# Kernel tuning notes

Measured on AMD Instinct MI355X. Metric: run time of the kernel, lower is better.

Reference implementation:

```python
import jax, jax.numpy as jnp
import numpy as np

K_HOPS = 4  # matches init kwarg K


def setup_inputs() -> dict:
    key = jax.random.key(0)
    ks = jax.random.split(key, 6)
    B, N, Fin, Fout = 32, 128, 64, 64
    x = jax.random.normal(ks[0], (B, N, Fin), dtype=jnp.float32)
    P = jax.random.normal(ks[1], (N, N), dtype=jnp.float32)
    Bb = jax.random.normal(ks[2], (N, 1), dtype=jnp.float32)
    Q = jax.random.normal(ks[3], (Fin, Fin), dtype=jnp.float32)
    T = jax.random.normal(ks[4], (Fin, N * Fin), dtype=jnp.float32)
    U = jax.random.normal(ks[5], (Fin, Fout), dtype=jnp.float32)
    return {"x": x, "P": P, "Bb": Bb, "Q": Q, "T": T, "U": U}


def reference(x, P, Bb, Q, T, U):
    B, N, Fin = x.shape
    # adjacency generation: O = P x + b, G = relu((O Q) T)
    O = jnp.matmul(P, x) + Bb                      # (B, N, Fin)
    G = jax.nn.relu(jnp.matmul(jnp.matmul(O, Q), T))  # (B, N, N*Fin)
    G = G.reshape(B, N, N, Fin).transpose(0, 3, 1, 2)  # (B, Fin, N, N)
    # degree normalization: A = diag(1/sqrt(colsum)) G diag(1/sqrt(rowsum))
    Dii = jnp.sqrt(jnp.sum(G, axis=-2))            # (B, Fin, N) column sums
    Djj = jnp.sqrt(jnp.sum(G, axis=-1))            # (B, Fin, N) row sums
    A = G / Dii[..., :, None] / Djj[..., None, :]  # (B, Fin, N, N)
    # K-hop power series: Asum = I + A + ... + A^{K-1}
    AA = jnp.broadcast_to(jnp.eye(N, dtype=x.dtype), A.shape)
    Asum = jnp.zeros_like(A)
    for _ in range(K_HOPS - 1):
        Asum = Asum + AA
        AA = jnp.matmul(A, AA)
    Asum = Asum + AA
    # propagate each feature channel: X[b,n,f] = sum_m Asum[b,f,n,m] x[b,m,f]
    Xf = jnp.einsum('bfnm,bmf->bnf', Asum, x)      # (B, N, Fin)
    return jnp.matmul(Xf, U)                       # (B, N, Fout)
```

## Files before the change

kernel.cpp:

```cpp
#include <hip/hip_runtime.h>


typedef __attribute__((ext_vector_type(8))) short short8v;
typedef __attribute__((ext_vector_type(4))) float f32x4;

#define WS_THE 0u
#define WS_TLE (1u << 20)
#define WS_XT  (2u << 20)
#define WS_TRE (3u << 20)
#define WS_OQH (3u << 20)
#define WS_OQL ((3u << 20) + (512u << 10))
#define WS_XFT (4u << 20)

__device__ __forceinline__ void split_bf16(float a, unsigned& hi, unsigned& lo) {
  unsigned ha = __float_as_uint(a) & 0xffff0000u;
  float d = a - __uint_as_float(ha);
  unsigned la = __float_as_uint(d) & 0xffff0000u;
  hi = ha; lo = la;
}

__global__ __launch_bounds__(256) void iag_k0_transpose(
    const float* __restrict__ T, const float* __restrict__ x,
    float* __restrict__ Tre, float* __restrict__ xT) {
  __shared__ float tile[64 * 65];
  int bi = blockIdx.x, tid = threadIdx.x;
  const float* src;
  float* dstbase;
  int fstride;
  if (bi < 128) {
    int k = bi >> 1, half = bi & 1;
    src = T + k * 8192 + half * 64 * 64;
    dstbase = Tre + k * 128 + half * 64;
    fstride = 8192;
  } else {
    int j = bi - 128;
    int b = j >> 1, half = j & 1;
    src = x + b * 8192 + half * 64 * 64;
    dstbase = xT + b * 8192 + half * 64;
    fstride = 128;
  }
  for (int idx = tid; idx < 4096; idx += 256) {
    int c = idx & 63, r = idx >> 6;
    tile[r * 65 + c] = src[idx];
  }
  __syncthreads();
  for (int idx = tid; idx < 4096; idx += 256) {
    int r = idx & 63, c = idx >> 6;
    dstbase[c * fstride + r] = tile[r * 65 + c];
  }
}

__global__ __launch_bounds__(256) void iag_k0b_split(
    const float* __restrict__ Tre, unsigned short* __restrict__ The,
    unsigned short* __restrict__ Tle) {
  __shared__ float tile[64 * 129];
  int f = blockIdx.x, tid = threadIdx.x;
  const float* src = Tre + f * 8192;
  for (int idx = tid; idx < 8192; idx += 256) {
    int k = idx >> 7, m = idx & 127;
    tile[k * 129 + m] = src[idx];
  }
  __syncthreads();
  int m = tid >> 1, kc = (tid & 1) * 32;
  unsigned hw[16], lw[16];
#pragma unroll
  for (int kk = 0; kk < 32; kk += 2) {
    float a0 = tile[(kc + kk) * 129 + m];
    float a1 = tile[(kc + kk + 1) * 129 + m];
    unsigned h0, l0, h1, l1;
    split_bf16(a0, h0, l0);
    split_bf16(a1, h1, l1);
    hw[kk >> 1] = (h0 >> 16) | h1;
    lw[kk >> 1] = (l0 >> 16) | l1;
  }
  uint4* dh = (uint4*)(The + f * 8192 + m * 64 + kc);
  uint4* dl = (uint4*)(Tle + f * 8192 + m * 64 + kc);
#pragma unroll
  for (int i = 0; i < 4; ++i) {
    dh[i] = make_uint4(hw[4 * i], hw[4 * i + 1], hw[4 * i + 2], hw[4 * i + 3]);
    dl[i] = make_uint4(lw[4 * i], lw[4 * i + 1], lw[4 * i + 2], lw[4 * i + 3]);
  }
}

__global__ __launch_bounds__(256) void iag_k1_oq(
    const float* __restrict__ x, const float* __restrict__ P,
    const float* __restrict__ Q, const float* __restrict__ Bb,
    unsigned short* __restrict__ OQh, unsigned short* __restrict__ OQl) {
  __shared__ __align__(16) float x_s[128 * 64];
  __shared__ float ptile[32 * 129];
  __shared__ __align__(16) float Q_s[64 * 64];
  __shared__ __align__(16) float OcT[64 * 32];
  int b = blockIdx.y, r0 = blockIdx.x * 32, tid = threadIdx.x;

  const float4* xg = (const float4*)(x + b * 8192);
  float4* xs4 = (float4*)x_s;
  for (int idx = tid; idx < 2048; idx += 256) xs4[idx] = xg[idx];
  for (int idx = tid; idx < 4096; idx += 256) {
    int nl = idx >> 7, m = idx & 127;
    ptile[nl * 129 + m] = P[(r0 + nl) * 128 + m];
  }
  const float4* qg = (const float4*)Q;
  float4* qs4 = (float4*)Q_s;
  for (int idx = tid; idx < 1024; idx += 256) qs4[idx] = qg[idx];
  __syncthreads();

  {
    int nl = tid & 31, k0 = (tid >> 5) * 8;
    float bias = Bb[r0 + nl];
    float a[8];
#pragma unroll
    for (int j = 0; j < 8; ++j) a[j] = bias;
#pragma unroll 4
    for (int m = 0; m < 128; ++m) {
      float p = ptile[nl * 129 + m];
      float4 x0 = xs4[m * 16 + (k0 >> 2)];
      float4 x1 = xs4[m * 16 + (k0 >> 2) + 1];
      a[0] += p * x0.x; a[1] += p * x0.y; a[2] += p * x0.z; a[3] += p * x0.w;
      a[4] += p * x1.x; a[5] += p * x1.y; a[6] += p * x1.z; a[7] += p * x1.w;
    }
#pragma unroll
    for (int j = 0; j < 8; ++j) OcT[(k0 + j) * 32 + nl] = a[j];
  }
  __syncthreads();
  {
    int nl = tid >> 3, j0 = (tid & 7) * 8;
    float c[8];
#pragma unroll
    for (int i = 0; i < 8; ++i) c[i] = 0.f;
    const float4* q4 = (const float4*)Q_s;
#pragma unroll 4
    for (int k = 0; k < 64; ++k) {
      float o = OcT[k * 32 + nl];
      float4 q0 = q4[k * 16 + (j0 >> 2)];
      float4 q1 = q4[k * 16 + (j0 >> 2) + 1];
      c[0] += o * q0.x; c[1] += o * q0.y; c[2] += o * q0.z; c[3] += o * q0.w;
      c[4] += o * q1.x; c[5] += o * q1.y; c[6] += o * q1.z; c[7] += o * q1.w;
    }
    unsigned hw[4], lw[4];
#pragma unroll
    for (int j = 0; j < 8; j += 2) {
      unsigned h0, l0, h1, l1;
      split_bf16(c[j], h0, l0);
      split_bf16(c[j + 1], h1, l1);
      hw[j >> 1] = (h0 >> 16) | h1;
      lw[j >> 1] = (l0 >> 16) | l1;
    }
    int n = r0 + nl;
    *(uint4*)(OQh + b * 8192 + n * 64 + j0) = make_uint4(hw[0], hw[1], hw[2], hw[3]);
    *(uint4*)(OQl + b * 8192 + n * 64 + j0) = make_uint4(lw[0], lw[1], lw[2], lw[3]);
  }
}

__global__ __launch_bounds__(256) void iag_k2_graph(
    const unsigned short* __restrict__ OQh, const unsigned short* __restrict__ OQl,
    const unsigned short* __restrict__ The, const unsigned short* __restrict__ Tle,
    const float* __restrict__ xT, float* __restrict__ Xft) {
  __shared__ unsigned short Ah[128 * 72], Al[128 * 72];
  __shared__ unsigned short Bh[128 * 72], Bl[128 * 72];
  __shared__ float red[4 * 128];
  __shared__ float invc[128], invr[128];
  __shared__ float wvb[2][128];
  int f = blockIdx.x, b = blockIdx.y, tid = threadIdx.x;

  {
    const unsigned short* sAh = OQh + b * 8192;
    const unsigned short* sAl = OQl + b * 8192;
    const unsigned short* sBh = The + f * 8192;
    const unsigned short* sBl = Tle + f * 8192;
#pragma unroll
    for (int it = 0; it < 4; ++it) {
      int c = tid + it * 256;
      int row = c >> 3, slot = c & 7;
      int so = row * 64 + slot * 8, dofs = row * 72 + slot * 8;
      *(uint4*)(Ah + dofs) = *(const uint4*)(sAh + so);
      *(uint4*)(Al + dofs) = *(const uint4*)(sAl + so);
      *(uint4*)(Bh + dofs) = *(const uint4*)(sBh + so);
      *(uint4*)(Bl + dofs) = *(const uint4*)(sBl + so);
    }
  }
  if (tid < 128) wvb[0][tid] = xT[(b * 64 + f) * 128 + tid];
  __syncthreads();

  int lane = tid & 63, w = tid >> 6;
  int li = lane & 15, lk = lane >> 4;

  short8v ah[2][2], al[2][2];
#pragma unroll
  for (int nt = 0; nt < 2; ++nt)
#pragma unroll
    for (int kh = 0; kh < 2; ++kh) {
      int off = (w * 32 + nt * 16 + li) * 72 + kh * 32 + lk * 8;
      ah[nt][kh] = *(const short8v*)((const short*)Ah + off);
      al[nt][kh] = *(const short8v*)((const short*)Al + off);
    }

  f32x4 acc[2][8];
#pragma unroll
  for (int nt = 0; nt < 2; ++nt)
#pragma unroll
    for (int mt = 0; mt < 8; ++mt) acc[nt][mt] = (f32x4){0.f, 0.f, 0.f, 0.f};

#pragma unroll
  for (int mt = 0; mt < 8; ++mt) {
    int off = (mt * 16 + li) * 72 + lk * 8;
    short8v bh0 = *(const short8v*)((const short*)Bh + off);
    short8v bh1 = *(const short8v*)((const short*)Bh + off + 32);
    short8v bl0 = *(const short8v*)((const short*)Bl + off);
    short8v bl1 = *(const short8v*)((const short*)Bl + off + 32);
#pragma unroll
    for (int nt = 0; nt < 2; ++nt) {
      f32x4 a = acc[nt][mt];
      a = __builtin_amdgcn_mfma_f32_16x16x32_bf16(ah[nt][0], bh0, a, 0, 0, 0);
      a = __builtin_amdgcn_mfma_f32_16x16x32_bf16(ah[nt][1], bh1, a, 0, 0, 0);
      a = __builtin_amdgcn_mfma_f32_16x16x32_bf16(ah[nt][0], bl0, a, 0, 0, 0);
      a = __builtin_amdgcn_mfma_f32_16x16x32_bf16(ah[nt][1], bl1, a, 0, 0, 0);
      a = __builtin_amdgcn_mfma_f32_16x16x32_bf16(al[nt][0], bh0, a, 0, 0, 0);
      a = __builtin_amdgcn_mfma_f32_16x16x32_bf16(al[nt][1], bh1, a, 0, 0, 0);
      acc[nt][mt] = a;
    }
  }

#pragma unroll
  for (int nt = 0; nt < 2; ++nt)
#pragma unroll
    for (int mt = 0; mt < 8; ++mt)
#pragma unroll
      for (int r = 0; r < 4; ++r) acc[nt][mt][r] = fmaxf(acc[nt][mt][r], 0.f);

#pragma unroll
  for (int mt = 0; mt < 8; ++mt) {
    float cs = 0.f;
#pragma unroll
    for (int nt = 0; nt < 2; ++nt)
#pragma unroll
      for (int r = 0; r < 4; ++r) cs += acc[nt][mt][r];
    cs += __shfl_xor(cs, 16);
    cs += __shfl_xor(cs, 32);
    if (lk == 0) red[w * 128 + mt * 16 + li] = cs;
  }
  {
    float rs[2][4];
#pragma unroll
    for (int nt = 0; nt < 2; ++nt)
#pragma unroll
      for (int r = 0; r < 4; ++r) {
        float s = 0.f;
#pragma unroll
        for (int mt = 0; mt < 8; ++mt) s += acc[nt][mt][r];
        rs[nt][r] = s;
      }
#pragma unroll
    for (int d = 1; d <= 8; d <<= 1)
#pragma unroll
      for (int nt = 0; nt < 2; ++nt)
#pragma unroll
        for (int r = 0; r < 4; ++r) rs[nt][r] += __shfl_xor(rs[nt][r], d);
    if (li == 0) {
#pragma unroll
      for (int nt = 0; nt < 2; ++nt)
#pragma unroll
        for (int r = 0; r < 4; ++r)
          invr[w * 32 + nt * 16 + lk * 4 + r] = rs[nt][r];
    }
  }
  __syncthreads();
  if (tid < 128) {
    float csum = red[tid] + red[128 + tid] + red[256 + tid] + red[384 + tid];
    invc[tid] = 1.0f / sqrtf(csum);
    invr[tid] = 1.0f / sqrtf(invr[tid]);
  }
  __syncthreads();

  {
    float icf[2][4], irf[8];
#pragma unroll
    for (int nt = 0; nt < 2; ++nt)
#pragma unroll
      for (int r = 0; r < 4; ++r) icf[nt][r] = invc[w * 32 + nt * 16 + lk * 4 + r];
#pragma unroll
    for (int mt = 0; mt < 8; ++mt) irf[mt] = invr[mt * 16 + li];
#pragma unroll
    for (int nt = 0; nt < 2; ++nt)
#pragma unroll
      for (int mt = 0; mt < 8; ++mt)
#pragma unroll
        for (int r = 0; r < 4; ++r) acc[nt][mt][r] *= icf[nt][r] * irf[mt];
  }

  float sv[2][4];
#pragma unroll
  for (int nt = 0; nt < 2; ++nt)
#pragma unroll
    for (int r = 0; r < 4; ++r) sv[nt][r] = wvb[0][w * 32 + nt * 16 + lk * 4 + r];
  int cur = 0;
  for (int h = 0; h < 3; ++h) {
    float wr[8];
#pragma unroll
    for (int mt = 0; mt < 8; ++mt) wr[mt] = wvb[cur][mt * 16 + li];
    float p[2][4];
#pragma unroll
    for (int nt = 0; nt < 2; ++nt)
#pragma unroll
      for (int r = 0; r < 4; ++r) {
        float s = 0.f;
#pragma unroll
        for (int mt = 0; mt < 8; ++mt) s += acc[nt][mt][r] * wr[mt];
        p[nt][r] = s;
      }
#pragma unroll
    for (int d = 1; d <= 8; d <<= 1)
#pragma unroll
      for (int nt = 0; nt < 2; ++nt)
#pragma unroll
        for (int r = 0; r < 4; ++r) p[nt][r] += __shfl_xor(p[nt][r], d);
#pragma unroll
    for (int nt = 0; nt < 2; ++nt)
#pragma unroll
      for (int r = 0; r < 4; ++r) sv[nt][r] += p[nt][r];
    if (li == 0) {
#pragma unroll
      for (int nt = 0; nt < 2; ++nt)
#pragma unroll
        for (int r = 0; r < 4; ++r)
          wvb[cur ^ 1][w * 32 + nt * 16 + lk * 4 + r] = p[nt][r];
    }
    __syncthreads();
    cur ^= 1;
  }
  if (li == 0) {
#pragma unroll
    for (int nt = 0; nt < 2; ++nt)
#pragma unroll
      for (int r = 0; r < 4; ++r)
        Xft[(b * 64 + f) * 128 + w * 32 + nt * 16 + lk * 4 + r] = sv[nt][r];
  }
}

__global__ __launch_bounds__(256) void iag_k3_out(
    const float* __restrict__ Xft, const float* __restrict__ U,
    float* __restrict__ out) {
  __shared__ float Xf_s[64 * 36];
  __shared__ __align__(16) float U_s[64 * 64];
  int b = blockIdx.y, n0 = blockIdx.x * 32, tid = threadIdx.x;
  for (int c = tid; c < 512; c += 256) {
    int ff = c >> 3, s = c & 7;
    float4 v = *(const float4*)(Xft + (b * 64 + ff) * 128 + n0 + s * 4);
    *(float4*)(Xf_s + ff * 36 + s * 4) = v;
  }
  const float4* ug = (const float4*)U;
  float4* us = (float4*)U_s;
  for (int c = tid; c < 1024; c += 256) us[c] = ug[c];
  __syncthreads();

  int j0 = (tid & 15) * 4, nl0 = (tid >> 4) * 2;
  float a0[4] = {0.f, 0.f, 0.f, 0.f}, a1[4] = {0.f, 0.f, 0.f, 0.f};
  const float4* u4 = (const float4*)U_s;
#pragma unroll 4
  for (int ff = 0; ff < 64; ++ff) {
    float4 u = u4[ff * 16 + (j0 >> 2)];
    float xa = Xf_s[ff * 36 + nl0];
    float xb = Xf_s[ff * 36 + nl0 + 1];
    a0[0] += xa * u.x; a0[1] += xa * u.y; a0[2] += xa * u.z; a0[3] += xa * u.w;
    a1[0] += xb * u.x; a1[1] += xb * u.y; a1[2] += xb * u.z; a1[3] += xb * u.w;
  }
  *(float4*)(out + b * 8192 + (n0 + nl0) * 64 + j0) =
      make_float4(a0[0], a0[1], a0[2], a0[3]);
  *(float4*)(out + b * 8192 + (n0 + nl0 + 1) * 64 + j0) =
      make_float4(a1[0], a1[1], a1[2], a1[3]);
}

extern "C" void kernel_launch(void* const* d_in, const int* in_sizes, int n_in,
                              void* d_out, int out_size, void* d_ws, size_t ws_size,
                              hipStream_t stream) {
  const float* x  = (const float*)d_in[0];
  const float* P  = (const float*)d_in[1];
  const float* Bb = (const float*)d_in[2];
  const float* Q  = (const float*)d_in[3];
  const float* T  = (const float*)d_in[4];
  const float* U  = (const float*)d_in[5];
  char* wsb = (char*)d_ws;
  unsigned short* The = (unsigned short*)(wsb + WS_THE);
  unsigned short* Tle = (unsigned short*)(wsb + WS_TLE);
  float* xT  = (float*)(wsb + WS_XT);
  float* Tre = (float*)(wsb + WS_TRE);
  unsigned short* OQh = (unsigned short*)(wsb + WS_OQH);
  unsigned short* OQl = (unsigned short*)(wsb + WS_OQL);
  float* Xft = (float*)(wsb + WS_XFT);

  iag_k0_transpose<<<192, 256, 0, stream>>>(T, x, Tre, xT);
  iag_k0b_split<<<64, 256, 0, stream>>>(Tre, The, Tle);
  iag_k1_oq<<<dim3(4, 32), 256, 0, stream>>>(x, P, Q, Bb, OQh, OQl);
  iag_k2_graph<<<dim3(64, 32), 256, 0, stream>>>(OQh, OQl, The, Tle, xT, Xft);
  iag_k3_out<<<dim3(4, 32), 256, 0, stream>>>(Xft, U, (float*)d_out);
}
```

Before: 123.2 us.

## Fuse preprocessing kernels and load MFMA operands directly from global memory

Merges the T transpose, the bf16 hi/lo split and the OQ computation into one preprocessing kernel, so the launch sequence drops from five kernels to three and the intermediate Tre and xT buffers go away. The graph kernel now reads its bf16 MFMA fragments straight from global memory instead of staging them in LDS, which removes the shared-memory copy and one barrier. It also gains a launch-bounds occupancy hint. The cost is repeated global or L2 fragment loads per wave and a strided global read of x for the propagation vector.

```diff
diff --git a/kernel.cpp b/kernel.cpp
--- a/kernel.cpp
+++ b/kernel.cpp
@@ -6,11 +6,9 @@
 
 #define WS_THE 0u
 #define WS_TLE (1u << 20)
-#define WS_XT  (2u << 20)
-#define WS_TRE (3u << 20)
-#define WS_OQH (3u << 20)
-#define WS_OQL ((3u << 20) + (512u << 10))
-#define WS_XFT (4u << 20)
+#define WS_OQH (2u << 20)
+#define WS_OQL ((2u << 20) + (512u << 10))
+#define WS_XFT (3u << 20)
 
 __device__ __forceinline__ void split_bf16(float a, unsigned& hi, unsigned& lo) {
   unsigned ha = __float_as_uint(a) & 0xffff0000u;
@@ -19,179 +17,139 @@
   hi = ha; lo = la;
 }
 
-__global__ __launch_bounds__(256) void iag_k0_transpose(
+__global__ __launch_bounds__(256) void iag_kpre(
     const float* __restrict__ T, const float* __restrict__ x,
-    float* __restrict__ Tre, float* __restrict__ xT) {
-  __shared__ float tile[64 * 65];
+    const float* __restrict__ P, const float* __restrict__ Q,
+    const float* __restrict__ Bb,
+    unsigned short* __restrict__ The, unsigned short* __restrict__ Tle,
+    unsigned short* __restrict__ OQh, unsigned short* __restrict__ OQl) {
+  __shared__ __align__(16) char smem[73856];
   int bi = blockIdx.x, tid = threadIdx.x;
-  const float* src;
-  float* dstbase;
-  int fstride;
-  if (bi < 128) {
-    int k = bi >> 1, half = bi & 1;
-    src = T + k * 8192 + half * 64 * 64;
-    dstbase = Tre + k * 128 + half * 64;
-    fstride = 8192;
+
+  if (bi < 64) {
+    float* tile = (float*)smem;
+    int m0 = bi * 2;
+    for (int idx = tid; idx < 8192; idx += 256) {
+      int k = idx >> 7, j = idx & 127;
+      tile[k * 129 + j] = T[k * 8192 + m0 * 64 + j];
+    }
+    __syncthreads();
+    int p = tid >> 1, kc = (tid & 1) * 32;
+    int fj = p & 63, ml = p >> 6;
+    int j = ml * 64 + fj;
+    unsigned hw[16], lw[16];
+#pragma unroll
+    for (int kk = 0; kk < 32; kk += 2) {
+      float a0 = tile[(kc + kk) * 129 + j];
+      float a1 = tile[(kc + kk + 1) * 129 + j];
+      unsigned h0, l0, h1, l1;
+      split_bf16(a0, h0, l0);
+      split_bf16(a1, h1, l1);
+      hw[kk >> 1] = (h0 >> 16) | h1;
+      lw[kk >> 1] = (l0 >> 16) | l1;
+    }
+    uint4* dh = (uint4*)(The + fj * 8192 + (m0 + ml) * 64 + kc);
+    uint4* dl = (uint4*)(Tle + fj * 8192 + (m0 + ml) * 64 + kc);
+#pragma unroll
+    for (int i = 0; i < 4; ++i) {
+      dh[i] = make_uint4(hw[4 * i], hw[4 * i + 1], hw[4 * i + 2], hw[4 * i + 3]);
+      dl[i] = make_uint4(lw[4 * i], lw[4 * i + 1], lw[4 * i + 2], lw[4 * i + 3]);
+    }
   } else {
-    int j = bi - 128;
-    int b = j >> 1, half = j & 1;
-    src = x + b * 8192 + half * 64 * 64;
-    dstbase = xT + b * 8192 + half * 64;
-    fstride = 128;
-  }
-  for (int idx = tid; idx < 4096; idx += 256) {
-    int c = idx & 63, r = idx >> 6;
-    tile[r * 65 + c] = src[idx];
-  }
-  __syncthreads();
-  for (int idx = tid; idx < 4096; idx += 256) {
-    int r = idx & 63, c = idx >> 6;
-    dstbase[c * fstride + r] = tile[r * 65 + c];
-  }
-}
-
-__global__ __launch_bounds__(256) void iag_k0b_split(
-    const float* __restrict__ Tre, unsigned short* __restrict__ The,
-    unsigned short* __restrict__ Tle) {
-  __shared__ float tile[64 * 129];
-  int f = blockIdx.x, tid = threadIdx.x;
-  const float* src = Tre + f * 8192;
-  for (int idx = tid; idx < 8192; idx += 256) {
-    int k = idx >> 7, m = idx & 127;
-    tile[k * 129 + m] = src[idx];
-  }
-  __syncthreads();
-  int m = tid >> 1, kc = (tid & 1) * 32;
-  unsigned hw[16], lw[16];
-#pragma unroll
-  for (int kk = 0; kk < 32; kk += 2) {
-    float a0 = tile[(kc + kk) * 129 + m];
-    float a1 = tile[(kc + kk + 1) * 129 + m];
-    unsigned h0, l0, h1, l1;
-    split_bf16(a0, h0, l0);
-    split_bf16(a1, h1, l1);
-    hw[kk >> 1] = (h0 >> 16) | h1;
-    lw[kk >> 1] = (l0 >> 16) | l1;
-  }
-  uint4* dh = (uint4*)(The + f * 8192 + m * 64 + kc);
-  uint4* dl = (uint4*)(Tle + f * 8192 + m * 64 + kc);
-#pragma unroll
-  for (int i = 0; i < 4; ++i) {
-    dh[i] = make_uint4(hw[4 * i], hw[4 * i + 1], hw[4 * i + 2], hw[4 * i + 3]);
-    dl[i] = make_uint4(lw[4 * i], lw[4 * i + 1], lw[4 * i + 2], lw[4 * i + 3]);
-  }
-}
-
-__global__ __launch_bounds__(256) void iag_k1_oq(
-    const float* __restrict__ x, const float* __restrict__ P,
-    const float* __restrict__ Q, const float* __restrict__ Bb,
-    unsigned short* __restrict__ OQh, unsigned short* __restrict__ OQl) {
-  __shared__ __align__(16) float x_s[128 * 64];
-  __shared__ float ptile[32 * 129];
-  __shared__ __align__(16) float Q_s[64 * 64];
-  __shared__ __align__(16) float OcT[64 * 32];
-  int b = blockIdx.y, r0 = blockIdx.x * 32, tid = threadIdx.x;
-
-  const float4* xg = (const float4*)(x + b * 8192);
-  float4* xs4 = (float4*)x_s;
-  for (int idx = tid; idx < 2048; idx += 256) xs4[idx] = xg[idx];
-  for (int idx = tid; idx < 4096; idx += 256) {
-    int nl = idx >> 7, m = idx & 127;
-    ptile[nl * 129 + m] = P[(r0 + nl) * 128 + m];
-  }
-  const float4* qg = (const float4*)Q;
-  float4* qs4 = (float4*)Q_s;
-  for (int idx = tid; idx < 1024; idx += 256) qs4[idx] = qg[idx];
-  __syncthreads();
-
-  {
-    int nl = tid & 31, k0 = (tid >> 5) * 8;
-    float bias = Bb[r0 + nl];
-    float a[8];
-#pragma unroll
-    for (int j = 0; j < 8; ++j) a[j] = bias;
+    float* x_s   = (float*)smem;
+    float* ptile = x_s + 128 * 64;
+    float* Q_s   = ptile + 32 * 129;
+    float* OcT   = Q_s + 64 * 64;
+    int jb = bi - 64;
+    int b = jb >> 2, r0 = (jb & 3) * 32;
+
+    const float4* xg = (const float4*)(x + b * 8192);
+    float4* xs4 = (float4*)x_s;
+    for (int idx = tid; idx < 2048; idx += 256) xs4[idx] = xg[idx];
+    for (int idx = tid; idx < 4096; idx += 256) {
+      int nl = idx >> 7, m = idx & 127;
+      ptile[nl * 129 + m] = P[(r0 + nl) * 128 + m];
+    }
+    const float4* qg = (const float4*)Q;
+    float4* qs4 = (float4*)Q_s;
+    for (int idx = tid; idx < 1024; idx += 256) qs4[idx] = qg[idx];
+    __syncthreads();
+
+    {
+      int nl = tid & 31, k0 = (tid >> 5) * 8;
+      float bias = Bb[r0 + nl];
+      float a[8];
+#pragma unroll
+      for (int j = 0; j < 8; ++j) a[j] = bias;
 #pragma unroll 4
-    for (int m = 0; m < 128; ++m) {
-      float p = ptile[nl * 129 + m];
-      float4 x0 = xs4[m * 16 + (k0 >> 2)];
-      float4 x1 = xs4[m * 16 + (k0 >> 2) + 1];
-      a[0] += p * x0.x; a[1] += p * x0.y; a[2] += p * x0.z; a[3] += p * x0.w;
-      a[4] += p * x1.x; a[5] += p * x1.y; a[6] += p * x1.z; a[7] += p * x1.w;
-    }
-#pragma unroll
-    for (int j = 0; j < 8; ++j) OcT[(k0 + j) * 32 + nl] = a[j];
-  }
-  __syncthreads();
-  {
-    int nl = tid >> 3, j0 = (tid & 7) * 8;
-    float c[8];
-#pragma unroll
-    for (int i = 0; i < 8; ++i) c[i] = 0.f;
-    const float4* q4 = (const float4*)Q_s;
+      for (int m = 0; m < 128; ++m) {
+        float p = ptile[nl * 129 + m];
+        float4 x0 = xs4[m * 16 + (k0 >> 2)];
+        float4 x1 = xs4[m * 16 + (k0 >> 2) + 1];
+        a[0] += p * x0.x; a[1] += p * x0.y; a[2] += p * x0.z; a[3] += p * x0.w;
+        a[4] += p * x1.x; a[5] += p * x1.y; a[6] += p * x1.z; a[7] += p * x1.w;
+      }
+#pragma unroll
+      for (int j = 0; j < 8; ++j) OcT[(k0 + j) * 32 + nl] = a[j];
+    }
+    __syncthreads();
+    {
+      int nl = tid >> 3, j0 = (tid & 7) * 8;
+      float c[8];
+#pragma unroll
+      for (int i = 0; i < 8; ++i) c[i] = 0.f;
+      const float4* q4 = (const float4*)Q_s;
 #pragma unroll 4
-    for (int k = 0; k < 64; ++k) {
-      float o = OcT[k * 32 + nl];
-      float4 q0 = q4[k * 16 + (j0 >> 2)];
-      float4 q1 = q4[k * 16 + (j0 >> 2) + 1];
-      c[0] += o * q0.x; c[1] += o * q0.y; c[2] += o * q0.z; c[3] += o * q0.w;
-      c[4] += o * q1.x; c[5] += o * q1.y; c[6] += o * q1.z; c[7] += o * q1.w;
-    }
-    unsigned hw[4], lw[4];
-#pragma unroll
-    for (int j = 0; j < 8; j += 2) {
-      unsigned h0, l0, h1, l1;
-      split_bf16(c[j], h0, l0);
-      split_bf16(c[j + 1], h1, l1);
-      hw[j >> 1] = (h0 >> 16) | h1;
-      lw[j >> 1] = (l0 >> 16) | l1;
-    }
-    int n = r0 + nl;
-    *(uint4*)(OQh + b * 8192 + n * 64 + j0) = make_uint4(hw[0], hw[1], hw[2], hw[3]);
-    *(uint4*)(OQl + b * 8192 + n * 64 + j0) = make_uint4(lw[0], lw[1], lw[2], lw[3]);
-  }
-}
-
-__global__ __launch_bounds__(256) void iag_k2_graph(
+      for (int k = 0; k < 64; ++k) {
+        float o = OcT[k * 32 + nl];
+        float4 q0 = q4[k * 16 + (j0 >> 2)];
+        float4 q1 = q4[k * 16 + (j0 >> 2) + 1];
+        c[0] += o * q0.x; c[1] += o * q0.y; c[2] += o * q0.z; c[3] += o * q0.w;
+        c[4] += o * q1.x; c[5] += o * q1.y; c[6] += o * q1.z; c[7] += o * q1.w;
+      }
+      unsigned hw[4], lw[4];
+#pragma unroll
+      for (int j = 0; j < 8; j += 2) {
+        unsigned h0, l0, h1, l1;
+        split_bf16(c[j], h0, l0);
+        split_bf16(c[j + 1], h1, l1);
+        hw[j >> 1] = (h0 >> 16) | h1;
+        lw[j >> 1] = (l0 >> 16) | l1;
+      }
+      int n = r0 + nl;
+      *(uint4*)(OQh + b * 8192 + n * 64 + j0) = make_uint4(hw[0], hw[1], hw[2], hw[3]);
+      *(uint4*)(OQl + b * 8192 + n * 64 + j0) = make_uint4(lw[0], lw[1], lw[2], lw[3]);
+    }
+  }
+}
+
+__global__ __launch_bounds__(256, 4) void iag_k2_graph(
     const unsigned short* __restrict__ OQh, const unsigned short* __restrict__ OQl,
     const unsigned short* __restrict__ The, const unsigned short* __restrict__ Tle,
-    const float* __restrict__ xT, float* __restrict__ Xft) {
-  __shared__ unsigned short Ah[128 * 72], Al[128 * 72];
-  __shared__ unsigned short Bh[128 * 72], Bl[128 * 72];
+    const float* __restrict__ x, float* __restrict__ Xft) {
   __shared__ float red[4 * 128];
   __shared__ float invc[128], invr[128];
   __shared__ float wvb[2][128];
   int f = blockIdx.x, b = blockIdx.y, tid = threadIdx.x;
 
-  {
-    const unsigned short* sAh = OQh + b * 8192;
-    const unsigned short* sAl = OQl + b * 8192;
-    const unsigned short* sBh = The + f * 8192;
-    const unsigned short* sBl = Tle + f * 8192;
-#pragma unroll
-    for (int it = 0; it < 4; ++it) {
-      int c = tid + it * 256;
-      int row = c >> 3, slot = c & 7;
-      int so = row * 64 + slot * 8, dofs = row * 72 + slot * 8;
-      *(uint4*)(Ah + dofs) = *(const uint4*)(sAh + so);
-      *(uint4*)(Al + dofs) = *(const uint4*)(sAl + so);
-      *(uint4*)(Bh + dofs) = *(const uint4*)(sBh + so);
-      *(uint4*)(Bl + dofs) = *(const uint4*)(sBl + so);
-    }
-  }
-  if (tid < 128) wvb[0][tid] = xT[(b * 64 + f) * 128 + tid];
-  __syncthreads();
+  if (tid < 128) wvb[0][tid] = x[b * 8192 + tid * 64 + f];
 
   int lane = tid & 63, w = tid >> 6;
   int li = lane & 15, lk = lane >> 4;
 
+  const unsigned short* Abh = OQh + b * 8192;
+  const unsigned short* Abl = OQl + b * 8192;
+  const unsigned short* Bbh = The + f * 8192;
+  const unsigned short* Bbl = Tle + f * 8192;
+
   short8v ah[2][2], al[2][2];
 #pragma unroll
   for (int nt = 0; nt < 2; ++nt)
 #pragma unroll
     for (int kh = 0; kh < 2; ++kh) {
-      int off = (w * 32 + nt * 16 + li) * 72 + kh * 32 + lk * 8;
-      ah[nt][kh] = *(const short8v*)((const short*)Ah + off);
-      al[nt][kh] = *(const short8v*)((const short*)Al + off);
+      int off = (w * 32 + nt * 16 + li) * 64 + kh * 32 + lk * 8;
+      ah[nt][kh] = *(const short8v*)(Abh + off);
+      al[nt][kh] = *(const short8v*)(Abl + off);
     }
 
   f32x4 acc[2][8];
@@ -202,11 +160,11 @@
 
 #pragma unroll
   for (int mt = 0; mt < 8; ++mt) {
-    int off = (mt * 16 + li) * 72 + lk * 8;
-    short8v bh0 = *(const short8v*)((const short*)Bh + off);
-    short8v bh1 = *(const short8v*)((const short*)Bh + off + 32);
-    short8v bl0 = *(const short8v*)((const short*)Bl + off);
-    short8v bl1 = *(const short8v*)((const short*)Bl + off + 32);
+    int off = (mt * 16 + li) * 64 + lk * 8;
+    short8v bh0 = *(const short8v*)(Bbh + off);
+    short8v bh1 = *(const short8v*)(Bbh + off + 32);
+    short8v bl0 = *(const short8v*)(Bbl + off);
+    short8v bl1 = *(const short8v*)(Bbl + off + 32);
 #pragma unroll
     for (int nt = 0; nt < 2; ++nt) {
       f32x4 a = acc[nt][mt];
@@ -381,15 +339,11 @@
   char* wsb = (char*)d_ws;
   unsigned short* The = (unsigned short*)(wsb + WS_THE);
   unsigned short* Tle = (unsigned short*)(wsb + WS_TLE);
-  float* xT  = (float*)(wsb + WS_XT);
-  float* Tre = (float*)(wsb + WS_TRE);
   unsigned short* OQh = (unsigned short*)(wsb + WS_OQH);
   unsigned short* OQl = (unsigned short*)(wsb + WS_OQL);
   float* Xft = (float*)(wsb + WS_XFT);
 
-  iag_k0_transpose<<<192, 256, 0, stream>>>(T, x, Tre, xT);
-  iag_k0b_split<<<64, 256, 0, stream>>>(Tre, The, Tle);
-  iag_k1_oq<<<dim3(4, 32), 256, 0, stream>>>(x, P, Q, Bb, OQh, OQl);
-  iag_k2_graph<<<dim3(64, 32), 256, 0, stream>>>(OQh, OQl, The, Tle, xT, Xft);
+  iag_kpre<<<192, 256, 0, stream>>>(T, x, P, Q, Bb, The, Tle, OQh, OQl);
+  iag_k2_graph<<<dim3(64, 32), 256, 0, stream>>>(OQh, OQl, The, Tle, x, Xft);
   iag_k3_out<<<dim3(4, 32), 256, 0, stream>>>(Xft, U, (float*)d_out);
 }
```

New measurement: 124.2 us. Within noise of the previous version (+0.9%).
